# Kernel optimization log

Measured on AMD Instinct MI355X. Metric: run time of the kernel, lower is better.

## Reference

```python
import jax, jax.numpy as jnp
import numpy as np
from jax import lax

# config constants (match init_kwargs)
SEQ_LEN = 512
PRED_LEN = 96
ENC_IN = 64
D_MODEL = 128
E_LAYERS = 2
GRAPH_SCALE = 16
GRAPH_RANK = 8
TCN_KERNEL = 3
TCN_DILATION = 2
BATCH = 16


def setup_inputs() -> dict:
    key = jax.random.key(0)
    ks = jax.random.split(key, 12)
    s = 0.02
    inp = {
        "x_enc": jax.random.normal(ks[0], (BATCH, SEQ_LEN, ENC_IN), jnp.float32),
        "x_mark_enc": jnp.zeros((BATCH, SEQ_LEN, 4), jnp.float32),
        "x_dec": jnp.zeros((BATCH, PRED_LEN, ENC_IN), jnp.float32),
        "x_mark_dec": jnp.zeros((BATCH, PRED_LEN, 4), jnp.float32),
        # value embedding (scalar -> d_model)
        "w_emb": jax.random.normal(ks[1], (1, D_MODEL), jnp.float32) * s,
        "b_emb": jnp.zeros((D_MODEL,), jnp.float32),
        # stacked dilated causal conv layers [L, K, Cin, Cout]
        "conv_w": jax.random.normal(ks[2], (E_LAYERS, TCN_KERNEL, D_MODEL, D_MODEL), jnp.float32) * s,
        "conv_b": jnp.zeros((E_LAYERS, D_MODEL), jnp.float32),
        # low-rank graph generator projections
        "gg_w1": jax.random.normal(ks[3], (D_MODEL, GRAPH_RANK), jnp.float32) * s,
        "gg_b1": jnp.zeros((GRAPH_RANK,), jnp.float32),
        "gg_w2": jax.random.normal(ks[4], (D_MODEL, GRAPH_RANK), jnp.float32) * s,
        "gg_b2": jnp.zeros((GRAPH_RANK,), jnp.float32),
        # head: Linear(d_model * num_tokens, pred_len)
        "head_w": jax.random.normal(ks[5], (D_MODEL * SEQ_LEN, PRED_LEN), jnp.float32) * s,
        "head_b": jnp.zeros((PRED_LEN,), jnp.float32),
    }
    return inp


def _tcn(x_enc, w_emb, b_emb, conv_w, conv_b):
    # x_enc: [B, L, N] -> channel-independent per-variable encoding -> [B, N, L, D]
    B, L, N = x_enc.shape
    h = x_enc.transpose(0, 2, 1).reshape(B * N, L, 1) @ w_emb + b_emb  # [B*N, L, D]
    for i in range(conv_w.shape[0]):
        dil = TCN_DILATION ** i
        pad = (TCN_KERNEL - 1) * dil
        hp = jnp.pad(h, ((0, 0), (pad, 0), (0, 0)))  # causal left pad
        y = lax.conv_general_dilated(
            hp, conv_w[i], window_strides=(1,), padding="VALID",
            rhs_dilation=(dil,), dimension_numbers=("NWC", "WIO", "NWC"),
        ) + conv_b[i]
        h = jax.nn.gelu(y) + h  # residual
    return h.reshape(B, N, L, -1)


def _forward(x_enc, w_emb, b_emb, conv_w, conv_b, gg_w1, gg_b1, gg_w2, gg_b2, head_w, head_b):
    h_time = _tcn(x_enc, w_emb, b_emb, conv_w, conv_b)  # [B, N, L, D]
    B, N, L, D = h_time.shape
    S = L // GRAPH_SCALE  # number of segments (L divisible by scale)
    h_seg = h_time.reshape(B, N, S, GRAPH_SCALE, D)
    z = h_seg.mean(axis=3)  # [B, N, S, D] segment summaries
    # low-rank graph generation for all segments at once
    e1 = z @ gg_w1 + gg_b1  # [B, N, S, r]
    e2 = z @ gg_w2 + gg_b2
    scores = jnp.einsum("bnsr,bmsr->bsnm", e1, e2) / jnp.asarray(np.sqrt(GRAPH_RANK), z.dtype)
    adj = jax.nn.softmax(scores, axis=-1)  # [B, S, N, N] row-stochastic
    # adjacency temporal-smoothness regularizer: sum_s mean|adj_s - adj_{s-1}|
    reg = jnp.sum(jnp.mean(jnp.abs(adj[:, 1:] - adj[:, :-1]), axis=(0, 2, 3)))
    # graph-weighted feature mixing per segment
    h_mix = jnp.einsum("bsnm,bmscd->bnscd", adj, h_seg).reshape(B, N, L, D)
    # head over flattened (token, dim)
    out = h_mix.reshape(B, N, L * D) @ head_w + head_b  # [B, N, pred_len]
    return out.transpose(0, 2, 1), reg  # [B, pred_len, N]


def reference(x_enc, x_mark_enc, x_dec, x_mark_dec, w_emb, b_emb, conv_w, conv_b,
              gg_w1, gg_b1, gg_w2, gg_b2, head_w, head_b):
    # x_mark_enc / x_dec / x_mark_dec are unused by forecast path (faithful to source)
    return _forward(x_enc, w_emb, b_emb, conv_w, conv_b, gg_w1, gg_b1, gg_w2, gg_b2, head_w, head_b)
```

## Files before the change

### kernel.cpp

```cpp
#include <hip/hip_runtime.h>
#include <hip/hip_bf16.h>


#define BATCH 16
#define SEQ 512
#define NVAR 64
#define DM 128
#define SEG 32
#define SCL 16
#define RNK 8
#define PRED 96
#define BN (BATCH * NVAR)
#define ROWLEN (SEQ * DM)

typedef unsigned short ushort_t;
typedef __attribute__((ext_vector_type(8))) short short8;
typedef __attribute__((ext_vector_type(4))) float f32x4;

__device__ inline float bf2f(ushort_t u) {
    union { unsigned int i; float f; } x;
    x.i = ((unsigned int)u) << 16;
    return x.f;
}
__device__ inline ushort_t f2bf(float f) {
    union { float f; unsigned int i; } u;
    u.f = f;
    unsigned int x = u.i;
    return (ushort_t)((x + 0x7fffu + ((x >> 16) & 1u)) >> 16);
}
__device__ inline unsigned int pkbf(float a, float b) {
    __hip_bfloat162 h = __float22bfloat162_rn(make_float2(a, b));
    union { __hip_bfloat162 h2; unsigned int u; } c;
    c.h2 = h;
    return c.u;
}
__device__ inline float blo(unsigned int u) {
    union { unsigned int i; float f; } x;
    x.i = u << 16;
    return x.f;
}
__device__ inline float bhi(unsigned int u) {
    union { unsigned int i; float f; } x;
    x.i = u & 0xFFFF0000u;
    return x.f;
}
__device__ inline float gelu_fast(float x) {
    float x2 = x * x;
    float t2 = x * fmaf(-0.10294854f, x2, -2.3022584f);
    float e;
    asm("v_exp_f32 %0, %1" : "=v"(e) : "v"(t2));
    return x * __builtin_amdgcn_rcpf(1.0f + e);
}

__global__ __launch_bounds__(128) void wt_prep(
    const float* __restrict__ conv_w, const float* __restrict__ w_emb,
    const float* __restrict__ b_emb, const float* __restrict__ conv_b,
    ushort_t* __restrict__ WTf, float* __restrict__ Acoef,
    float* __restrict__ Bias3, float* __restrict__ regacc) {
    if (blockIdx.x == 0 && blockIdx.y == 0 && threadIdx.x == 0) regacc[0] = 0.f;
    if (blockIdx.x < 3) {
        int tap = blockIdx.x;
        int ci = blockIdx.y;
        int co = threadIdx.x;
        int kt = ci >> 5, quad = (ci >> 3) & 3, j = ci & 7;
        int ng = co >> 4, col = co & 15;
        int lane = quad * 16 + col;
        WTf[((((size_t)tap * 4 + kt) * 8 + ng) * 64 + lane) * 8 + j] =
            f2bf(conv_w[(size_t)(3 + tap) * 16384 + (size_t)ci * 128 + co]);
    } else if (blockIdx.y == 0) {
        int co = threadIdx.x;
        float a0 = 0.f, a1 = 0.f, a2 = 0.f, c0 = 0.f, c1 = 0.f, c2 = 0.f;
        for (int ci = 0; ci < 128; ++ci) {
            float we = w_emb[ci], be = b_emb[ci];
            float w0 = conv_w[((size_t)(0 * 128 + ci)) * 128 + co];
            float w1 = conv_w[((size_t)(1 * 128 + ci)) * 128 + co];
            float w2 = conv_w[((size_t)(2 * 128 + ci)) * 128 + co];
            a0 += we * w0; c0 += be * w0;
            a1 += we * w1; c1 += be * w1;
            a2 += we * w2; c2 += be * w2;
        }
        Acoef[0 * 128 + co] = a0;
        Acoef[1 * 128 + co] = a1;
        Acoef[2 * 128 + co] = a2;
        float b0 = conv_b[co];
        Bias3[0 * 128 + co] = b0 + c2;
        Bias3[1 * 128 + co] = b0 + c1 + c2;
        Bias3[2 * 128 + co] = b0 + c0 + c1 + c2;
    }
}

__global__ __launch_bounds__(256) void hw_prep(
    const float* __restrict__ head_w, ushort_t* __restrict__ HWf, int kh) {
    __shared__ float ts[32 * 97];
    int k32p = blockIdx.x;
    int s = k32p >> 5, t = k32p & 31;
    int kbase = (s * 64 + kh * 32 + t) * 32;
    const float* src = head_w + (size_t)kbase * 96;
    for (int idx = threadIdx.x; idx < 3072; idx += 256) {
        int kk = idx / 96, p = idx - kk * 96;
        ts[kk * 97 + p] = src[idx];
    }
    __syncthreads();
    unsigned int* ob32 =
        reinterpret_cast<unsigned int*>(HWf + (size_t)k32p * 3072);
    for (int odx = threadIdx.x; odx < 1536; odx += 256) {
        int p = odx >> 4, kk = (odx & 15) * 2;
        ob32[odx] = pkbf(ts[kk * 97 + p], ts[(kk + 1) * 97 + p]);
    }
}

__global__ __launch_bounds__(256, 4) void tcn_mfma(
    const float* __restrict__ x, const float* __restrict__ w_emb,
    const float* __restrict__ b_emb, const float* __restrict__ Acoef,
    const float* __restrict__ Bias3, const ushort_t* __restrict__ WTf,
    const float* __restrict__ conv_b,
    const float* __restrict__ gw1, const float* __restrict__ gb1,
    const float* __restrict__ gw2, const float* __restrict__ gb2,
    ushort_t* __restrict__ h2, float* __restrict__ e1, float* __restrict__ e2) {
    __shared__ __align__(16) ushort_t h1s[68 * 136];
    __shared__ float xs[70];
    __shared__ float zbuf[4 * 128];

    int bn = blockIdx.x;
    int b = bn >> 6, n = bn & 63;
    int chunk = blockIdx.y;
    int l0 = chunk * 64;
    int tid = threadIdx.x;

    {
        const float* xb = x + (size_t)b * SEQ * NVAR + n;
        if (tid < 70) {
            int l = l0 - 6 + tid;
            xs[tid] = (l >= 0) ? xb[(size_t)l * NVAR] : 0.0f;
        }
    }
    __syncthreads();

    {
        int dp = (tid & 63) * 2;
        float2 A0 = *reinterpret_cast<const float2*>(&Acoef[0 * 128 + dp]);
        float2 A1 = *reinterpret_cast<const float2*>(&Acoef[1 * 128 + dp]);
        float2 A2 = *reinterpret_cast<const float2*>(&Acoef[2 * 128 + dp]);
        float2 BF = *reinterpret_cast<const float2*>(&Bias3[2 * 128 + dp]);
        float2 we2 = *reinterpret_cast<const float2*>(&w_emb[dp]);
        float2 be2 = *reinterpret_cast<const float2*>(&b_emb[dp]);
#pragma unroll
        for (int i = 0; i < 17; ++i) {
            int row = (tid >> 6) + 4 * i;
            int l = l0 - 4 + row;
            unsigned int pk = 0;
            if (l >= 0) {
                float x0 = xs[row], x1 = xs[row + 1], x2 = xs[row + 2];
                float2 bias = BF;
                if (l < 2)
                    bias = *reinterpret_cast<const float2*>(&Bias3[l * 128 + dp]);
                float y0 = fmaf(x0, A0.x, fmaf(x1, A1.x, fmaf(x2, A2.x, bias.x)));
                float y1 = fmaf(x0, A0.y, fmaf(x1, A1.y, fmaf(x2, A2.y, bias.y)));
                float r0 = gelu_fast(y0) + fmaf(x2, we2.x, be2.x);
                float r1 = gelu_fast(y1) + fmaf(x2, we2.y, be2.y);
                pk = pkbf(r0, r1);
            }
            *reinterpret_cast<unsigned int*>(&h1s[row * 136 + dp]) = pk;
        }
    }
    __syncthreads();

    int lane = tid & 63;
    int wv = tid >> 6;
    int quad = lane >> 4;
    int col = lane & 15;
    int cobase = wv * 32;

    f32x4 acc2[4][2];
#pragma unroll
    for (int mt = 0; mt < 4; ++mt)
#pragma unroll
        for (int nt = 0; nt < 2; ++nt)
            acc2[mt][nt] = (f32x4){0.f, 0.f, 0.f, 0.f};

#pragma unroll
    for (int tap = 0; tap < 3; ++tap) {
        short8 wf0[4], wf1[4];
#pragma unroll
        for (int kt = 0; kt < 4; ++kt) {
            const ushort_t* bp =
                WTf + ((((size_t)tap * 4 + kt) * 8 + wv * 2) * 64 + lane) * 8;
            wf0[kt] = *(const short8*)bp;
            wf1[kt] = *(const short8*)(bp + 512);
        }
#pragma unroll
        for (int kt = 0; kt < 4; ++kt) {
            int kc = kt * 32 + quad * 8;
#pragma unroll
            for (int mt = 0; mt < 4; ++mt) {
                short8 hf = *(const short8*)&h1s[(mt * 16 + col + 2 * tap) * 136 + kc];
                acc2[mt][0] = __builtin_amdgcn_mfma_f32_16x16x32_bf16(wf0[kt], hf, acc2[mt][0], 0, 0, 0);
                acc2[mt][1] = __builtin_amdgcn_mfma_f32_16x16x32_bf16(wf1[kt], hf, acc2[mt][1], 0, 0, 0);
            }
        }
    }

    {
        uint2 res[4][2];
#pragma unroll
        for (int mt = 0; mt < 4; ++mt) {
            int li = mt * 16 + col;
#pragma unroll
            for (int nt = 0; nt < 2; ++nt) {
                int co = cobase + nt * 16 + quad * 4;
                res[mt][nt] = *reinterpret_cast<const uint2*>(
                    &h1s[(li + 4) * 136 + co]);
            }
        }
        __syncthreads();
        float4 bias[2];
        bias[0] = *reinterpret_cast<const float4*>(&conv_b[DM + cobase + quad * 4]);
        bias[1] = *reinterpret_cast<const float4*>(&conv_b[DM + cobase + 16 + quad * 4]);
#pragma unroll
        for (int mt = 0; mt < 4; ++mt) {
            int li = mt * 16 + col;
#pragma unroll
            for (int nt = 0; nt < 2; ++nt) {
                int co = cobase + nt * 16 + quad * 4;
                float h0 = gelu_fast(acc2[mt][nt][0] + bias[nt].x) + blo(res[mt][nt].x);
                float h1 = gelu_fast(acc2[mt][nt][1] + bias[nt].y) + bhi(res[mt][nt].x);
                float h2v = gelu_fast(acc2[mt][nt][2] + bias[nt].z) + blo(res[mt][nt].y);
                float h3 = gelu_fast(acc2[mt][nt][3] + bias[nt].w) + bhi(res[mt][nt].y);
                uint2 pk;
                pk.x = pkbf(h0, h1);
                pk.y = pkbf(h2v, h3);
                *reinterpret_cast<uint2*>(&h1s[li * 136 + co]) = pk;
            }
        }
    }
    __syncthreads();

    {
        ushort_t* orow = h2 + (size_t)bn * ROWLEN + (size_t)l0 * 128;
#pragma unroll
        for (int i = 0; i < 4; ++i) {
            int q = tid + 256 * i;
            int row = q >> 4, c8 = (q & 15) * 8;
            *(short8*)&orow[row * 128 + c8] = *(const short8*)&h1s[row * 136 + c8];
        }
    }
    {
        int d = tid & 127, sg = tid >> 7;
#pragma unroll
        for (int t = 0; t < 2; ++t) {
            int sl = sg + 2 * t;
            float a = 0.0f;
#pragma unroll
            for (int c = 0; c < SCL; ++c)
                a += bf2f(h1s[(sl * 16 + c) * 136 + d]);
            zbuf[sl * 128 + d] = a * (1.0f / 16.0f);
        }
    }
    __syncthreads();
    {
        int out = tid >> 2;
        int part = tid & 3;
        int sl = out >> 4;
        int which = (out >> 3) & 1;
        int r = out & 7;
        const float* w = which ? gw2 : gw1;
        float a = 0.0f;
        int d0 = part * 32;
        for (int d = d0; d < d0 + 32; ++d)
            a += zbuf[sl * 128 + d] * w[d * RNK + r];
        a += __shfl_xor(a, 1, 64);
        a += __shfl_xor(a, 2, 64);
        if (part == 0) {
            a += (which ? gb2 : gb1)[r];
            int s = chunk * 4 + sl;
            (which ? e2 : e1)[(((size_t)b * SEG + s) * NVAR + n) * RNK + r] = a;
        }
    }
}

__global__ __launch_bounds__(256) void g_gemm(
    const ushort_t* __restrict__ h2, const ushort_t* __restrict__ HWf,
    float* __restrict__ G, int kh, int first) {
    __shared__ __align__(16) ushort_t As[2][64 * 72];
    int s = blockIdx.x;
    int bnt = blockIdx.y;
    int bn0 = bnt * 64;
    int kbase = kh * 1024;
    int lane = threadIdx.x & 63, wv = threadIdx.x >> 6;
    int quad = lane >> 4, col = lane & 15;
    int mh = wv & 1;
    int ph = wv >> 1;
    int p0 = ph * 48 + col;

    int arow = threadIdx.x >> 2, akq = (threadIdx.x & 3) * 16;
    const ushort_t* aptr =
        h2 + (size_t)(bn0 + arow) * ROWLEN + (size_t)s * 2048 + kbase + akq;
    const ushort_t* hb =
        HWf + (size_t)s * 98304 + (size_t)p0 * 32 + quad * 8;

    f32x4 acc[3][2];
#pragma unroll
    for (int i = 0; i < 3; ++i)
#pragma unroll
        for (int j = 0; j < 2; ++j) acc[i][j] = (f32x4){0.f, 0.f, 0.f, 0.f};

    short8 pa0 = *(const short8*)aptr;
    short8 pa1 = *(const short8*)(aptr + 8);
    short8 pf[2][2][3];
#pragma unroll
    for (int kk = 0; kk < 2; ++kk)
#pragma unroll
        for (int i = 0; i < 3; ++i)
            pf[0][kk][i] = *(const short8*)(hb + kk * 3072 + i * 512);
    *(short8*)&As[0][arow * 72 + akq] = pa0;
    *(short8*)&As[0][arow * 72 + akq + 8] = pa1;
    __syncthreads();

#pragma unroll
    for (int kt = 0; kt < 16; ++kt) {
        const int par = kt & 1;
        if (kt < 15) {
            const ushort_t* ap = aptr + (kt + 1) * 64;
            pa0 = *(const short8*)ap;
            pa1 = *(const short8*)(ap + 8);
            const ushort_t* fb = hb + (size_t)(kt + 1) * 6144;
#pragma unroll
            for (int kk = 0; kk < 2; ++kk)
#pragma unroll
                for (int i = 0; i < 3; ++i)
                    pf[par ^ 1][kk][i] =
                        *(const short8*)(fb + kk * 3072 + i * 512);
        }
#pragma unroll
        for (int kk = 0; kk < 2; ++kk) {
            int kc = kk * 32 + quad * 8;
#pragma unroll
            for (int j = 0; j < 2; ++j) {
                short8 bnfr =
                    *(const short8*)&As[par][(mh * 32 + j * 16 + col) * 72 + kc];
#pragma unroll
                for (int i = 0; i < 3; ++i)
                    acc[i][j] = __builtin_amdgcn_mfma_f32_16x16x32_bf16(
                        pf[par][kk][i], bnfr, acc[i][j], 0, 0, 0);
            }
        }
        if (kt < 15) {
            *(short8*)&As[par ^ 1][arow * 72 + akq] = pa0;
            *(short8*)&As[par ^ 1][arow * 72 + akq + 8] = pa1;
        }
        __syncthreads();
    }

#pragma unroll
    for (int i = 0; i < 3; ++i)
#pragma unroll
        for (int j = 0; j < 2; ++j)
#pragma unroll
            for (int r = 0; r < 4; ++r) {
                int p = ph * 48 + i * 16 + quad * 4 + r;
                int m = mh * 32 + j * 16 + col;
                size_t o = (((size_t)s * BATCH + bnt) * PRED + p) * NVAR + m;
                if (first) G[o] = acc[i][j][r];
                else G[o] += acc[i][j][r];
            }
}

__global__ __launch_bounds__(256) void out_partial(
    const float* __restrict__ e1, const float* __restrict__ e2,
    const float* __restrict__ G, float* __restrict__ partial,
    float* __restrict__ regacc) {
    __shared__ float adjn[2][32][65];
    __shared__ float Gs[96][65];
    __shared__ float e2s[3][64][8];
    __shared__ float e1s[3][32][8];
    __shared__ float wsum[4];
    int b = blockIdx.x, sg = blockIdx.y, nh = blockIdx.z;
    int s0 = sg * 2;
    int wv = threadIdx.x >> 6, lane = threadIdx.x & 63;

    for (int idx = threadIdx.x; idx < 3 * 64 * 8; idx += 256) {
        int j = idx >> 9, m = (idx >> 3) & 63, r = idx & 7;
        int s = s0 - 1 + j;
        e2s[j][m][r] = (s >= 0)
            ? e2[(((size_t)b * SEG + s) * NVAR + m) * RNK + r] : 0.0f;
    }
    for (int idx = threadIdx.x; idx < 3 * 32 * 8; idx += 256) {
        int j = idx >> 8, nl = (idx >> 3) & 31, r = idx & 7;
        int s = s0 - 1 + j;
        e1s[j][nl][r] = (s >= 0)
            ? e1[(((size_t)b * SEG + s) * NVAR + nh * 32 + nl) * RNK + r] : 0.0f;
    }
    __syncthreads();

    float regsum = 0.0f;
    for (int t = 0; t < 8; ++t) {
        int nl = wv * 8 + t;
        float a[3];
#pragma unroll
        for (int j = 0; j < 3; ++j) {
            float sc = 0.0f;
#pragma unroll
            for (int r = 0; r < 8; ++r) sc += e1s[j][nl][r] * e2s[j][lane][r];
            sc *= 0.35355339059327373f;
            float mx = sc;
            for (int off = 32; off; off >>= 1)
                mx = fmaxf(mx, __shfl_xor(mx, off, 64));
            float ex = __expf(sc - mx);
            float sm = ex;
            for (int off = 32; off; off >>= 1) sm += __shfl_xor(sm, off, 64);
            a[j] = ex * __builtin_amdgcn_rcpf(sm);
        }
        if (s0 > 0) regsum += fabsf(a[1] - a[0]);
        regsum += fabsf(a[2] - a[1]);
        adjn[0][nl][lane] = a[1];
        adjn[1][nl][lane] = a[2];
    }
    __syncthreads();

    int pg = threadIdx.x >> 4;
    int ng = threadIdx.x & 15;
    float acc[6][2];
#pragma unroll
    for (int j = 0; j < 6; ++j) { acc[j][0] = 0.f; acc[j][1] = 0.f; }

#pragma unroll
    for (int ss = 0; ss < 2; ++ss) {
        int s = s0 + ss;
#pragma unroll
        for (int i = 0; i < 6; ++i) {
            int q = threadIdx.x + 256 * i;
            int row = q >> 4, mq = (q & 15) * 4;
            float4 v = *reinterpret_cast<const float4*>(
                &G[(((size_t)s * BATCH + b) * PRED + row) * NVAR + mq]);
            Gs[row][mq + 0] = v.x; Gs[row][mq + 1] = v.y;
            Gs[row][mq + 2] = v.z; Gs[row][mq + 3] = v.w;
        }
        __syncthreads();
#pragma unroll 4
        for (int m = 0; m < 64; ++m) {
            float a0 = adjn[ss][ng * 2 + 0][m];
            float a1 = adjn[ss][ng * 2 + 1][m];
#pragma unroll
            for (int j = 0; j < 6; ++j) {
                float g = Gs[pg * 6 + j][m];
                acc[j][0] += g * a0;
                acc[j][1] += g * a1;
            }
        }
        __syncthreads();
    }
#pragma unroll
    for (int j = 0; j < 6; ++j)
#pragma unroll
        for (int i = 0; i < 2; ++i) {
            int p = pg * 6 + j, n = nh * 32 + ng * 2 + i;
            partial[(((size_t)sg * BATCH + b) * PRED + p) * NVAR + n] = acc[j][i];
        }
    for (int off = 32; off; off >>= 1) regsum += __shfl_xor(regsum, off, 64);
    if (lane == 0) wsum[wv] = regsum;
    __syncthreads();
    if (threadIdx.x == 0)
        atomicAdd(regacc, wsum[0] + wsum[1] + wsum[2] + wsum[3]);
}

__global__ __launch_bounds__(256) void out_reduce(
    const float* __restrict__ partial, const float* __restrict__ head_b,
    const float* __restrict__ regacc, float* __restrict__ out, int out_size) {
    int i4 = blockIdx.x * 256 + threadIdx.x;
    int p = (i4 >> 4) % PRED;
    float hb = head_b[p];
    float4 a = make_float4(hb, hb, hb, hb);
    const int stride4 = BATCH * PRED * NVAR / 4;
    const float4* p4 = reinterpret_cast<const float4*>(partial);
#pragma unroll
    for (int sg = 0; sg < 16; ++sg) {
        float4 v = p4[sg * stride4 + i4];
        a.x += v.x; a.y += v.y; a.z += v.z; a.w += v.w;
    }
    reinterpret_cast<float4*>(out)[i4] = a;
    if (i4 == 0) out[out_size - 1] = regacc[0] * (1.0f / 65536.0f);
}

extern "C" void kernel_launch(void* const* d_in, const int* in_sizes, int n_in,
                              void* d_out, int out_size, void* d_ws,
                              size_t ws_size, hipStream_t stream) {
    const float* x_enc  = (const float*)d_in[0];
    const float* w_emb  = (const float*)d_in[4];
    const float* b_emb  = (const float*)d_in[5];
    const float* conv_w = (const float*)d_in[6];
    const float* conv_b = (const float*)d_in[7];
    const float* gg_w1  = (const float*)d_in[8];
    const float* gg_b1  = (const float*)d_in[9];
    const float* gg_w2  = (const float*)d_in[10];
    const float* gg_b2  = (const float*)d_in[11];
    const float* head_w = (const float*)d_in[12];
    const float* head_b = (const float*)d_in[13];
    float* out = (float*)d_out;

    char* ws = (char*)d_ws;
    ushort_t* h2   = (ushort_t*)(ws);
    float* partial = (float*)(ws);
    float* G       = (float*)(ws + 134217728);
    float* e1      = (float*)(ws + 146800640);
    float* e2      = (float*)(ws + 147849216);
    ushort_t* WTf  = (ushort_t*)(ws + 148897792);
    float* Acoef   = (float*)(ws + 148996096);
    float* Bias3   = (float*)(ws + 148997632);
    ushort_t* HWf  = (ushort_t*)(ws + 149000192);
    float* regacc  = (float*)(ws + 157286400);

    wt_prep<<<dim3(4, 128), 128, 0, stream>>>(
        conv_w, w_emb, b_emb, conv_b, WTf, Acoef, Bias3, regacc);
    tcn_mfma<<<dim3(BN, SEQ / 64), 256, 0, stream>>>(
        x_enc, w_emb, b_emb, Acoef, Bias3, WTf, conv_b,
        gg_w1, gg_b1, gg_w2, gg_b2, h2, e1, e2);
    hw_prep<<<1024, 256, 0, stream>>>(head_w, HWf, 0);
    g_gemm<<<dim3(SEG, BATCH), 256, 0, stream>>>(h2, HWf, G, 0, 1);
    hw_prep<<<1024, 256, 0, stream>>>(head_w, HWf, 1);
    g_gemm<<<dim3(SEG, BATCH), 256, 0, stream>>>(h2, HWf, G, 1, 0);
    out_partial<<<dim3(BATCH, 16, 2), 256, 0, stream>>>(
        e1, e2, G, partial, regacc);
    out_reduce<<<BATCH * PRED * NVAR / 1024, 256, 0, stream>>>(
        partial, head_b, regacc, out, out_size);
}
```

Before: 297.1 us.

## Merge prep kernels, atomically accumulate output, and vectorize segment-mean reduction

Folds the conv-weight prep, the first head-weight bf16 repack and an output bias initialisation into one prep launch. The mixing kernel now atomically adds its per-segment-group results straight into the output instead of writing partials for a separate reduce kernel, which becomes a one-thread finaliser for the regulariser. The segment mean in the TCN kernel reads packed bf16 pairs, and the graph projection interleaves the d index across the four partial lanes with a padded buffer. This saves launches and partial-buffer traffic but adds float atomic contention (16 adds per output) and makes the summation order nondeterministic.

```diff
diff --git a/kernel.cpp b/kernel.cpp
--- a/kernel.cpp
+++ b/kernel.cpp
@@ -52,40 +52,68 @@
     return x * __builtin_amdgcn_rcpf(1.0f + e);
 }
 
-__global__ __launch_bounds__(128) void wt_prep(
+__global__ __launch_bounds__(256) void prep(
     const float* __restrict__ conv_w, const float* __restrict__ w_emb,
     const float* __restrict__ b_emb, const float* __restrict__ conv_b,
+    const float* __restrict__ head_w, const float* __restrict__ head_b,
     ushort_t* __restrict__ WTf, float* __restrict__ Acoef,
-    float* __restrict__ Bias3, float* __restrict__ regacc) {
-    if (blockIdx.x == 0 && blockIdx.y == 0 && threadIdx.x == 0) regacc[0] = 0.f;
-    if (blockIdx.x < 3) {
-        int tap = blockIdx.x;
-        int ci = blockIdx.y;
-        int co = threadIdx.x;
-        int kt = ci >> 5, quad = (ci >> 3) & 3, j = ci & 7;
-        int ng = co >> 4, col = co & 15;
-        int lane = quad * 16 + col;
-        WTf[((((size_t)tap * 4 + kt) * 8 + ng) * 64 + lane) * 8 + j] =
-            f2bf(conv_w[(size_t)(3 + tap) * 16384 + (size_t)ci * 128 + co]);
-    } else if (blockIdx.y == 0) {
-        int co = threadIdx.x;
-        float a0 = 0.f, a1 = 0.f, a2 = 0.f, c0 = 0.f, c1 = 0.f, c2 = 0.f;
-        for (int ci = 0; ci < 128; ++ci) {
-            float we = w_emb[ci], be = b_emb[ci];
-            float w0 = conv_w[((size_t)(0 * 128 + ci)) * 128 + co];
-            float w1 = conv_w[((size_t)(1 * 128 + ci)) * 128 + co];
-            float w2 = conv_w[((size_t)(2 * 128 + ci)) * 128 + co];
-            a0 += we * w0; c0 += be * w0;
-            a1 += we * w1; c1 += be * w1;
-            a2 += we * w2; c2 += be * w2;
-        }
-        Acoef[0 * 128 + co] = a0;
-        Acoef[1 * 128 + co] = a1;
-        Acoef[2 * 128 + co] = a2;
-        float b0 = conv_b[co];
-        Bias3[0 * 128 + co] = b0 + c2;
-        Bias3[1 * 128 + co] = b0 + c1 + c2;
-        Bias3[2 * 128 + co] = b0 + c0 + c1 + c2;
+    float* __restrict__ Bias3, ushort_t* __restrict__ HWf,
+    float* __restrict__ out, float* __restrict__ regacc) {
+    __shared__ float ts[32 * 97];
+    int bid = blockIdx.x;
+    if (bid == 0 && threadIdx.x == 0) regacc[0] = 0.f;
+    if (bid < 512) {
+        int bx = bid >> 7, ci = bid & 127;
+        if (threadIdx.x < 128) {
+            int co = threadIdx.x;
+            if (bx < 3) {
+                int kt = ci >> 5, quad = (ci >> 3) & 3, j = ci & 7;
+                int ng = co >> 4, col = co & 15;
+                int lane = quad * 16 + col;
+                WTf[((((size_t)bx * 4 + kt) * 8 + ng) * 64 + lane) * 8 + j] =
+                    f2bf(conv_w[(size_t)(3 + bx) * 16384 + (size_t)ci * 128 + co]);
+            } else if (ci == 0) {
+                float a0 = 0.f, a1 = 0.f, a2 = 0.f, c0 = 0.f, c1 = 0.f, c2 = 0.f;
+                for (int k = 0; k < 128; ++k) {
+                    float we = w_emb[k], be = b_emb[k];
+                    float w0 = conv_w[((size_t)(0 * 128 + k)) * 128 + co];
+                    float w1 = conv_w[((size_t)(1 * 128 + k)) * 128 + co];
+                    float w2 = conv_w[((size_t)(2 * 128 + k)) * 128 + co];
+                    a0 += we * w0; c0 += be * w0;
+                    a1 += we * w1; c1 += be * w1;
+                    a2 += we * w2; c2 += be * w2;
+                }
+                Acoef[0 * 128 + co] = a0;
+                Acoef[1 * 128 + co] = a1;
+                Acoef[2 * 128 + co] = a2;
+                float b0 = conv_b[co];
+                Bias3[0 * 128 + co] = b0 + c2;
+                Bias3[1 * 128 + co] = b0 + c1 + c2;
+                Bias3[2 * 128 + co] = b0 + c0 + c1 + c2;
+            }
+        }
+    } else if (bid < 1536) {
+        int k32p = bid - 512;
+        int s = k32p >> 5, t = k32p & 31;
+        int kbase = (s * 64 + t) * 32;
+        const float* src = head_w + (size_t)kbase * 96;
+        for (int idx = threadIdx.x; idx < 3072; idx += 256) {
+            int kk = idx / 96, p = idx - kk * 96;
+            ts[kk * 97 + p] = src[idx];
+        }
+        __syncthreads();
+        unsigned int* ob32 =
+            reinterpret_cast<unsigned int*>(HWf + (size_t)k32p * 3072);
+        for (int odx = threadIdx.x; odx < 1536; odx += 256) {
+            int p = odx >> 4, kk = (odx & 15) * 2;
+            ob32[odx] = pkbf(ts[kk * 97 + p], ts[(kk + 1) * 97 + p]);
+        }
+    } else {
+        int idx = (bid - 1536) * 256 + threadIdx.x;
+        if (idx < BATCH * PRED * NVAR) {
+            int p = (idx >> 6) % PRED;
+            out[idx] = head_b[p];
+        }
     }
 }
 
@@ -119,7 +147,7 @@
     ushort_t* __restrict__ h2, float* __restrict__ e1, float* __restrict__ e2) {
     __shared__ __align__(16) ushort_t h1s[68 * 136];
     __shared__ float xs[70];
-    __shared__ float zbuf[4 * 128];
+    __shared__ float zbuf[4 * 136];
 
     int bn = blockIdx.x;
     int b = bn >> 6, n = bn & 63;
@@ -245,29 +273,33 @@
         }
     }
     {
-        int d = tid & 127, sg = tid >> 7;
-#pragma unroll
-        for (int t = 0; t < 2; ++t) {
-            int sl = sg + 2 * t;
-            float a = 0.0f;
-#pragma unroll
-            for (int c = 0; c < SCL; ++c)
-                a += bf2f(h1s[(sl * 16 + c) * 136 + d]);
-            zbuf[sl * 128 + d] = a * (1.0f / 16.0f);
-        }
+        int sl = tid >> 6;
+        int dp = (tid & 63) * 2;
+        float a0 = 0.0f, a1 = 0.0f;
+#pragma unroll
+        for (int c = 0; c < SCL; ++c) {
+            unsigned int u = *reinterpret_cast<const unsigned int*>(
+                &h1s[(sl * 16 + c) * 136 + dp]);
+            a0 += blo(u);
+            a1 += bhi(u);
+        }
+        zbuf[sl * 136 + dp] = a0 * 0.0625f;
+        zbuf[sl * 136 + dp + 1] = a1 * 0.0625f;
     }
     __syncthreads();
     {
-        int out = tid >> 2;
+        int outi = tid >> 2;
         int part = tid & 3;
-        int sl = out >> 4;
-        int which = (out >> 3) & 1;
-        int r = out & 7;
+        int sl = outi >> 4;
+        int which = (outi >> 3) & 1;
+        int r = outi & 7;
         const float* w = which ? gw2 : gw1;
         float a = 0.0f;
-        int d0 = part * 32;
-        for (int d = d0; d < d0 + 32; ++d)
-            a += zbuf[sl * 128 + d] * w[d * RNK + r];
+#pragma unroll 8
+        for (int i = 0; i < 32; ++i) {
+            int d = i * 4 + part;
+            a += zbuf[sl * 136 + d] * w[d * RNK + r];
+        }
         a += __shfl_xor(a, 1, 64);
         a += __shfl_xor(a, 2, 64);
         if (part == 0) {
@@ -365,9 +397,9 @@
             }
 }
 
-__global__ __launch_bounds__(256) void out_partial(
+__global__ __launch_bounds__(256) void out_mix(
     const float* __restrict__ e1, const float* __restrict__ e2,
-    const float* __restrict__ G, float* __restrict__ partial,
+    const float* __restrict__ G, float* __restrict__ out,
     float* __restrict__ regacc) {
     __shared__ float adjn[2][32][65];
     __shared__ float Gs[96][65];
@@ -454,7 +486,7 @@
 #pragma unroll
         for (int i = 0; i < 2; ++i) {
             int p = pg * 6 + j, n = nh * 32 + ng * 2 + i;
-            partial[(((size_t)sg * BATCH + b) * PRED + p) * NVAR + n] = acc[j][i];
+            atomicAdd(&out[((size_t)b * PRED + p) * NVAR + n], acc[j][i]);
         }
     for (int off = 32; off; off >>= 1) regsum += __shfl_xor(regsum, off, 64);
     if (lane == 0) wsum[wv] = regsum;
@@ -463,22 +495,9 @@
         atomicAdd(regacc, wsum[0] + wsum[1] + wsum[2] + wsum[3]);
 }
 
-__global__ __launch_bounds__(256) void out_reduce(
-    const float* __restrict__ partial, const float* __restrict__ head_b,
-    const float* __restrict__ regacc, float* __restrict__ out, int out_size) {
-    int i4 = blockIdx.x * 256 + threadIdx.x;
-    int p = (i4 >> 4) % PRED;
-    float hb = head_b[p];
-    float4 a = make_float4(hb, hb, hb, hb);
-    const int stride4 = BATCH * PRED * NVAR / 4;
-    const float4* p4 = reinterpret_cast<const float4*>(partial);
-#pragma unroll
-    for (int sg = 0; sg < 16; ++sg) {
-        float4 v = p4[sg * stride4 + i4];
-        a.x += v.x; a.y += v.y; a.z += v.z; a.w += v.w;
-    }
-    reinterpret_cast<float4*>(out)[i4] = a;
-    if (i4 == 0) out[out_size - 1] = regacc[0] * (1.0f / 65536.0f);
+__global__ void fin(const float* __restrict__ regacc, float* __restrict__ out,
+                    int out_size) {
+    out[out_size - 1] = regacc[0] * (1.0f / 65536.0f);
 }
 
 extern "C" void kernel_launch(void* const* d_in, const int* in_sizes, int n_in,
@@ -499,7 +518,6 @@
 
     char* ws = (char*)d_ws;
     ushort_t* h2   = (ushort_t*)(ws);
-    float* partial = (float*)(ws);
     float* G       = (float*)(ws + 134217728);
     float* e1      = (float*)(ws + 146800640);
     float* e2      = (float*)(ws + 147849216);
@@ -509,17 +527,16 @@
     ushort_t* HWf  = (ushort_t*)(ws + 149000192);
     float* regacc  = (float*)(ws + 157286400);
 
-    wt_prep<<<dim3(4, 128), 128, 0, stream>>>(
-        conv_w, w_emb, b_emb, conv_b, WTf, Acoef, Bias3, regacc);
+    prep<<<1920, 256, 0, stream>>>(
+        conv_w, w_emb, b_emb, conv_b, head_w, head_b,
+        WTf, Acoef, Bias3, HWf, out, regacc);
     tcn_mfma<<<dim3(BN, SEQ / 64), 256, 0, stream>>>(
         x_enc, w_emb, b_emb, Acoef, Bias3, WTf, conv_b,
         gg_w1, gg_b1, gg_w2, gg_b2, h2, e1, e2);
-    hw_prep<<<1024, 256, 0, stream>>>(head_w, HWf, 0);
     g_gemm<<<dim3(SEG, BATCH), 256, 0, stream>>>(h2, HWf, G, 0, 1);
     hw_prep<<<1024, 256, 0, stream>>>(head_w, HWf, 1);
     g_gemm<<<dim3(SEG, BATCH), 256, 0, stream>>>(h2, HWf, G, 1, 0);
-    out_partial<<<dim3(BATCH, 16, 2), 256, 0, stream>>>(
-        e1, e2, G, partial, regacc);
-    out_reduce<<<BATCH * PRED * NVAR / 1024, 256, 0, stream>>>(
-        partial, head_b, regacc, out, out_size);
-}
+    out_mix<<<dim3(BATCH, 16, 2), 256, 0, stream>>>(
+        e1, e2, G, out, regacc);
+    fin<<<1, 1, 0, stream>>>(regacc, out, out_size);
+}
```

New measurement: 292.5 us, median of 3. No clear change (-1.6%).
